# Optimization experiments

Measured on AMD Instinct MI355X. Metric: run time of the kernel, lower is better.

Reference implementation:

```python
import jax, jax.numpy as jnp
import numpy as np

DIM, HEADS, EMB = 768, 16, 1024
DH = DIM // HEADS                 # 48, divisible by 3 for 3D RoPE
T, RES = 3, 24
KT, KH, KW = 3, 5, 5              # neighborhood kernel
MLP = 4 * DIM
EPS = 1e-5


def _ln(x, w=None, b=None):
    m = x.mean(-1, keepdims=True)
    v = x.var(-1, keepdims=True)
    y = (x - m) * jax.lax.rsqrt(v + EPS)
    if w is not None:
        y = y * w + b
    return y


def _rope_cos_sin():
    # 3D axial RoPE: dim_head split into 3 equal chunks (t, h, w axes)
    da = DH // 3
    half = da // 2
    inv = 1.0 / (10000.0 ** (jnp.arange(half, dtype=jnp.float32) * 2.0 / da))
    def ang(n):
        return jnp.arange(n, dtype=jnp.float32)[:, None] * inv[None, :]  # (n, half)
    at, ah, aw = ang(T), ang(RES), ang(RES)
    A = jnp.concatenate([
        jnp.broadcast_to(at[:, None, None, :], (T, RES, RES, half)),
        jnp.broadcast_to(ah[None, :, None, :], (T, RES, RES, half)),
        jnp.broadcast_to(aw[None, None, :, :], (T, RES, RES, half)),
    ], axis=-1).reshape(T * RES * RES, DH // 2)
    return jnp.cos(A), jnp.sin(A)


def _rope(x, cos, sin):  # x: (B, nh, THW, DH); interleaved pair rotation
    x1, x2 = x[..., 0::2], x[..., 1::2]
    o1 = x1 * cos - x2 * sin
    o2 = x1 * sin + x2 * cos
    return jnp.stack([o1, o2], axis=-1).reshape(x.shape)


def _nbr(n, k):
    # NATTEN window: centered, shifted inward at borders (always exactly k neighbors)
    start = jnp.clip(jnp.arange(n) - k // 2, 0, n - k)
    return start[:, None] + jnp.arange(k)  # (n, k)


def setup_inputs():
    key = jax.random.key(0)
    ks = jax.random.split(key, 8)
    r = lambda k, s: jax.random.normal(k, s, dtype=jnp.float32) * 0.02
    return {
        "x": jax.random.normal(ks[0], (T, DIM, RES, RES), dtype=jnp.float32),
        "emb": jax.random.normal(ks[1], (T, EMB), dtype=jnp.float32),
        "w_mod": r(ks[2], (EMB, 2 * DIM)),
        "b_mod": jnp.zeros((2 * DIM,), jnp.float32),
        "qn_w": jnp.ones((DH,), jnp.float32),
        "qn_b": jnp.zeros((DH,), jnp.float32),
        "kn_w": jnp.ones((DH,), jnp.float32),
        "kn_b": jnp.zeros((DH,), jnp.float32),
        "W_fused": r(ks[3], (DIM, 3 * DIM + MLP)),
        "b_fused": jnp.zeros((3 * DIM + MLP,), jnp.float32),
        "W_out": r(ks[4], (DIM, DIM)),
        "W_mlp": r(ks[5], (MLP, DIM)),
        "b_mlp": jnp.zeros((DIM,), jnp.float32),
    }


def reference(x, emb, w_mod, b_mod, qn_w, qn_b, kn_w, kn_b,
              W_fused, b_fused, W_out, W_mlp, b_mlp):
    B = x.shape[0] // T
    H = W = RES
    THW = T * H * W
    x5 = x.reshape(B, T, DIM, H, W)
    skip = jnp.transpose(x5, (0, 1, 3, 4, 2))          # (B,T,H,W,C)
    xf = skip.reshape(B, THW, DIM)
    # conditioning emb repeated over spatial positions
    embr = jnp.repeat(emb.reshape(B, T, EMB)[:, :, None, :], H * W, axis=2)
    embr = embr.reshape(B, THW, EMB)
    # NormalizeWithCond: LayerNorm (no affine) + AdaLN modulation from emb
    mod = jax.nn.silu(embr) @ w_mod + b_mod
    scale, shift = jnp.split(mod, 2, axis=-1)
    h = _ln(xf) * (1.0 + scale) + shift
    # fused QKV + MLP projection
    fused = h @ W_fused + b_fused
    qkv, mlp_h = fused[..., :3 * DIM], fused[..., 3 * DIM:]
    qkv = qkv.reshape(B, THW, 3, HEADS, DH).transpose(2, 0, 3, 1, 4)  # (3,B,nh,THW,d)
    q, k, v = qkv[0], qkv[1], qkv[2]
    q = _ln(q, qn_w, qn_b)
    k = _ln(k, kn_w, kn_b)
    cos, sin = _rope_cos_sin()
    q = _rope(q, cos, sin)
    k = _rope(k, cos, sin)
    q = q.reshape(B, HEADS, T, H, W, DH) * (DH ** -0.5)
    k = k.reshape(B, HEADS, T, H, W, DH)
    v = v.reshape(B, HEADS, T, H, W, DH)
    it, ih, iw = _nbr(T, KT), _nbr(H, KH), _nbr(W, KW)
    def gather(z):  # -> (B,nh,T,KT,H,KH,W,KW,d)
        return z[:, :, it][:, :, :, :, ih][:, :, :, :, :, :, iw]
    kg, vg = gather(k), gather(v)
    attn = jnp.einsum('bnthwd,bntahcwed->bnthwace', q, kg)
    attn = jax.nn.softmax(attn.reshape(B, HEADS, T, H, W, KT * KH * KW), axis=-1)
    attn = attn.reshape(B, HEADS, T, H, W, KT, KH, KW)
    xa = jnp.einsum('bnthwace,bntahcwed->bnthwd', attn, vg)
    xa = jnp.transpose(xa, (0, 2, 3, 4, 1, 5)).reshape(B, T, H, W, DIM)
    y = skip + xa @ W_out
    y = y.reshape(B, THW, DIM) + (jax.nn.silu(mlp_h) @ W_mlp + b_mlp)
    y = jnp.transpose(y.reshape(B, T, H, W, DIM), (0, 1, 4, 2, 3))
    return y.reshape(B * T, DIM, H, W)
```

## Files before the change

kernel.cpp:

```cpp
#include <hip/hip_runtime.h>
#include <hip/hip_bf16.h>
#include <math.h>

#define T_    3
#define RES_  24
#define DIM_  768
#define HEADS_ 16
#define DH_   48
#define EMB_  1024
#define HW_   576
#define THW_  1728
#define MP_   1792
#define MLP_  3072
#define NF_   5376
#define QKV_  2304
#define KTOT_ 3840
#define SPLITK_ 6
#define EPS_  1e-5f

typedef __attribute__((ext_vector_type(8))) short bf16x8;
typedef __attribute__((ext_vector_type(4))) float f32x4;

__device__ __forceinline__ float siluf(float x) { return x / (1.f + expf(-x)); }

__device__ __forceinline__ unsigned short f2bf(float f) {
    __hip_bfloat16 b = __float2bfloat16(f);
    return *reinterpret_cast<unsigned short*>(&b);
}

__device__ __forceinline__ float bf2f(unsigned short u) {
    return __uint_as_float(((unsigned)u) << 16);
}

__device__ __forceinline__ void async_copy16(const void* g, void* l) {
    __builtin_amdgcn_global_load_lds(
        (__attribute__((address_space(1))) void*)g,
        (__attribute__((address_space(3))) void*)l,
        16, 0, 0);
}

__global__ __launch_bounds__(256) void conv_wfused_kernel(
    const float* __restrict__ W, unsigned short* __restrict__ Wt)
{
    __shared__ float tile[32][33];
    int n0 = blockIdx.x * 32;
    int k0 = blockIdx.y * 32;
    int c = threadIdx.x & 31;
    int r = threadIdx.x >> 5;
#pragma unroll
    for (int i = 0; i < 4; ++i)
        tile[r + 8 * i][c] = W[(size_t)(k0 + r + 8 * i) * NF_ + n0 + c];
    __syncthreads();
#pragma unroll
    for (int i = 0; i < 4; ++i)
        Wt[(size_t)(n0 + r + 8 * i) * DIM_ + k0 + c] = f2bf(tile[c][r + 8 * i]);
}

__global__ __launch_bounds__(256) void conv_wcat_kernel(
    const float* __restrict__ W_out, const float* __restrict__ W_mlp,
    unsigned short* __restrict__ Wt)
{
    __shared__ float tile[32][33];
    int k0 = blockIdx.x * 32;
    int n0 = blockIdx.y * 32;
    int c = threadIdx.x & 31;
    int r = threadIdx.x >> 5;
#pragma unroll
    for (int i = 0; i < 4; ++i) {
        int k = k0 + r + 8 * i;
        float v = (k < DIM_) ? W_out[(size_t)k * DIM_ + n0 + c]
                             : W_mlp[(size_t)(k - DIM_) * DIM_ + n0 + c];
        tile[r + 8 * i][c] = v;
    }
    __syncthreads();
#pragma unroll
    for (int i = 0; i < 4; ++i)
        Wt[(size_t)(n0 + r + 8 * i) * KTOT_ + k0 + c] = f2bf(tile[c][r + 8 * i]);
}

__global__ __launch_bounds__(256) void mod_kernel(
    const float* __restrict__ emb, const float* __restrict__ w_mod,
    const float* __restrict__ b_mod, float* __restrict__ mod)
{
    int t = blockIdx.y;
    int chunk = blockIdx.x;
    __shared__ float se[EMB_];
    __shared__ float part[128];
    int tid = threadIdx.x;
    for (int i = tid; i < EMB_; i += 256) {
        float e = emb[t * EMB_ + i];
        se[i] = e / (1.f + expf(-e));
    }
    __syncthreads();
    int r = tid >> 7;
    int c = tid & 127;
    int j = chunk * 128 + c;
    const float* wp = w_mod + j;
    float acc = 0.f;
    for (int e = r * 512; e < r * 512 + 512; ++e)
        acc += se[e] * wp[e * 1536];
    if (r == 1) part[c] = acc;
    __syncthreads();
    if (r == 0)
        mod[t * 1536 + j] = acc + part[c] + b_mod[j];
}

__global__ __launch_bounds__(256) void ln_mod_kernel(
    const float* __restrict__ x, const float* __restrict__ mod,
    unsigned short* __restrict__ h)
{
    int m = blockIdx.x;
    int t = m / HW_;
    int hw = m - t * HW_;
    const float* xp = x + (size_t)t * DIM_ * HW_ + hw;
    int tid = threadIdx.x;
    float v0 = xp[(size_t)tid * HW_];
    float v1 = xp[(size_t)(tid + 256) * HW_];
    float v2 = xp[(size_t)(tid + 512) * HW_];
    float s  = v0 + v1 + v2;
    float sq = v0 * v0 + v1 * v1 + v2 * v2;
#pragma unroll
    for (int off = 32; off > 0; off >>= 1) {
        s  += __shfl_xor(s, off, 64);
        sq += __shfl_xor(sq, off, 64);
    }
    __shared__ float ssum[4], ssq[4];
    int lane = tid & 63, wid = tid >> 6;
    if (lane == 0) { ssum[wid] = s; ssq[wid] = sq; }
    __syncthreads();
    float tot  = ssum[0] + ssum[1] + ssum[2] + ssum[3];
    float totq = ssq[0] + ssq[1] + ssq[2] + ssq[3];
    float mean = tot * (1.f / 768.f);
    float var  = totq * (1.f / 768.f) - mean * mean;
    float rs = rsqrtf(var + EPS_);
    const float* sc = mod + t * 1536;
    const float* sh = sc + 768;
    unsigned short* hp = h + (size_t)m * DIM_;
    hp[tid]       = f2bf((v0 - mean) * rs * (1.f + sc[tid])       + sh[tid]);
    hp[tid + 256] = f2bf((v1 - mean) * rs * (1.f + sc[tid + 256]) + sh[tid + 256]);
    hp[tid + 512] = f2bf((v2 - mean) * rs * (1.f + sc[tid + 512]) + sh[tid + 512]);
}

__global__ __launch_bounds__(256) void gemm1_kernel(
    const unsigned short* __restrict__ A,
    const unsigned short* __restrict__ Bt,
    const float* __restrict__ bias,
    float* __restrict__ qkv,
    unsigned short* __restrict__ A2)
{
    const int K = DIM_;
    __shared__ unsigned short As[128 * 32];
    __shared__ unsigned short Bs[128 * 32];
    int tid = threadIdx.x;
    int bm = blockIdx.y * 128;
    int bn = blockIdx.x * 128;
    int wave = tid >> 6, lane = tid & 63;
    int quad = lane >> 4, l16 = lane & 15;
    int wm = (wave & 1) * 64;
    int wn = (wave >> 1) * 64;
    f32x4 acc[4][4] = {};
    int srow = tid >> 2;
    int skk  = (tid & 3) * 8;
    const unsigned short* Ag = A + (size_t)(bm + srow) * K + skk;
    const unsigned short* Bg = Bt + (size_t)(bn + srow) * K + skk;
    unsigned short* la0 = &As[srow * 32 + skk];
    unsigned short* la1 = &As[(srow + 64) * 32 + skk];
    unsigned short* lb0 = &Bs[srow * 32 + skk];
    unsigned short* lb1 = &Bs[(srow + 64) * 32 + skk];
    for (int k0 = 0; k0 < K; k0 += 32) {
        async_copy16(Ag + k0, la0);
        async_copy16(Ag + (size_t)64 * K + k0, la1);
        async_copy16(Bg + k0, lb0);
        async_copy16(Bg + (size_t)64 * K + k0, lb1);
        __syncthreads();
        bf16x8 af[4], bf[4];
#pragma unroll
        for (int mt = 0; mt < 4; ++mt)
            af[mt] = *(const bf16x8*)&As[(wm + mt * 16 + l16) * 32 + quad * 8];
#pragma unroll
        for (int nt = 0; nt < 4; ++nt)
            bf[nt] = *(const bf16x8*)&Bs[(wn + nt * 16 + l16) * 32 + quad * 8];
#pragma unroll
        for (int mt = 0; mt < 4; ++mt)
#pragma unroll
            for (int nt = 0; nt < 4; ++nt)
                acc[mt][nt] = __builtin_amdgcn_mfma_f32_16x16x32_bf16(
                    af[mt], bf[nt], acc[mt][nt], 0, 0, 0);
        __syncthreads();
    }
#pragma unroll
    for (int mt = 0; mt < 4; ++mt) {
#pragma unroll
        for (int nt = 0; nt < 4; ++nt) {
            int gcol = bn + wn + nt * 16 + l16;
            float b = bias[gcol];
#pragma unroll
            for (int r = 0; r < 4; ++r) {
                int grow = bm + wm + mt * 16 + quad * 4 + r;
                if (grow < THW_) {
                    float v = acc[mt][nt][r] + b;
                    if (gcol < QKV_)
                        qkv[(size_t)grow * QKV_ + gcol] = v;
                    else
                        A2[(size_t)grow * KTOT_ + (gcol - QKV_ + DIM_)] = f2bf(siluf(v));
                }
            }
        }
    }
}

__global__ __launch_bounds__(256) void qkln_rope_kernel(
    const float* __restrict__ qkv,
    const float* __restrict__ qn_w, const float* __restrict__ qn_b,
    const float* __restrict__ kn_w, const float* __restrict__ kn_b,
    float* __restrict__ qb, float* __restrict__ kb)
{
    int tid = threadIdx.x;
    int lane = tid & 63, wid = tid >> 6;
    int idx = blockIdx.x * 4 + wid;
    int head = idx / THW_;
    int m = idx - head * THW_;
    const float* fp = qkv + (size_t)m * QKV_ + head * DH_;
    float qv = 0.f, kv = 0.f;
    if (lane < DH_) { qv = fp[lane]; kv = fp[768 + lane]; }
    float s = qv, sq = qv * qv, sk = kv, sqk = kv * kv;
#pragma unroll
    for (int off = 32; off > 0; off >>= 1) {
        s   += __shfl_xor(s, off, 64);
        sq  += __shfl_xor(sq, off, 64);
        sk  += __shfl_xor(sk, off, 64);
        sqk += __shfl_xor(sqk, off, 64);
    }
    float mq = s  * (1.f / 48.f), vq = sq  * (1.f / 48.f) - mq * mq;
    float mk = sk * (1.f / 48.f), vk = sqk * (1.f / 48.f) - mk * mk;
    float qn = 0.f, kn = 0.f;
    if (lane < DH_) {
        qn = (qv - mq) * rsqrtf(vq + EPS_) * qn_w[lane] + qn_b[lane];
        kn = (kv - mk) * rsqrtf(vk + EPS_) * kn_w[lane] + kn_b[lane];
    }
    int t = m / HW_; int hw = m - t * HW_;
    int hh = hw / RES_; int ww = hw - hh * RES_;
    int i = lane >> 1;
    int grp = i >> 3, j = i & 7;
    float pos = (grp == 0) ? (float)t : (grp == 1) ? (float)hh : (float)ww;
    float invf = exp2f(-1.6609640474436813f * (float)j);
    float ang = pos * invf;
    float cs = cosf(ang), sn = sinf(ang);
    float qp = __shfl_xor(qn, 1, 64);
    float kp = __shfl_xor(kn, 1, 64);
    float qo, ko;
    if ((lane & 1) == 0) { qo = qn * cs - qp * sn; ko = kn * cs - kp * sn; }
    else                 { qo = qp * sn + qn * cs; ko = kp * sn + kn * cs; }
    if (lane < DH_) {
        size_t o = ((size_t)head * THW_ + m) * DH_ + lane;
        qb[o] = qo * 0.14433756729740643f;
        kb[o] = ko;
    }
}

__global__ __launch_bounds__(256) void attn_kernel(
    const float* __restrict__ qb, const float* __restrict__ kb,
    const float* __restrict__ qkv, unsigned short* __restrict__ A2)
{
    __shared__ unsigned short Ks[144 * 72];
    __shared__ unsigned short Vt[48 * 168];
    __shared__ unsigned short Ps[64 * 168];

    int tid = threadIdx.x;
    int lane = tid & 63, wave = tid >> 6;
    int quad = lane >> 4, l16 = lane & 15;

    int head = blockIdx.x / 27;
    int tile = blockIdx.x - head * 27;
    int tt = tile / 9;
    int sp = tile - tt * 9;
    int h0 = (sp / 3) * 8;
    int w0 = (sp - (sp / 3) * 3) * 8;
    int u0h = min(max(h0 - 2, 0), RES_ - 12);
    int u0w = min(max(w0 - 2, 0), RES_ - 12);

    const float* qbh = qb + (size_t)head * THW_ * DH_;
    const float* kbh = kb + (size_t)head * THW_ * DH_;

    for (int i = tid; i < 144 * 24; i += 256) {
        int r = i / 24;
        Ks[r * 72 + 48 + (i - r * 24)] = 0;
    }
    for (int i = tid; i < 48 * 24; i += 256) {
        int r = i / 24;
        Vt[r * 168 + 144 + (i - r * 24)] = 0;
    }
    for (int i = tid; i < 64 * 24; i += 256) {
        int r = i / 24;
        Ps[r * 168 + 144 + (i - r * 24)] = 0;
    }

    int qbase = wave * 16;
    bf16x8 qf0, qf1;
    {
        int g = qbase + l16;
        int qtok = tt * HW_ + (h0 + (g >> 3)) * RES_ + (w0 + (g & 7));
        const float* qp = qbh + (size_t)qtok * DH_;
#pragma unroll
        for (int i = 0; i < 8; ++i) qf0[i] = (short)f2bf(qp[quad * 8 + i]);
        if (quad < 2) {
#pragma unroll
            for (int i = 0; i < 8; ++i) qf1[i] = (short)f2bf(qp[32 + quad * 8 + i]);
        } else {
#pragma unroll
            for (int i = 0; i < 8; ++i) qf1[i] = 0;
        }
    }

    int vmask[4];
#pragma unroll
    for (int r = 0; r < 4; ++r) {
        int g = qbase + quad * 4 + r;
        int qh = h0 + (g >> 3), qw = w0 + (g & 7);
        int hs = min(max(qh - 2, 0), RES_ - 5);
        int ws = min(max(qw - 2, 0), RES_ - 5);
        int vm = 0;
#pragma unroll
        for (int nt = 0; nt < 9; ++nt) {
            int kk = nt * 16 + l16;
            int hc = u0h + kk / 12;
            int wc = u0w + kk - (kk / 12) * 12;
            int ok = (hc >= hs) & (hc < hs + 5) & (wc >= ws) & (wc < ws + 5);
            vm |= ok << nt;
        }
        vmask[r] = vm;
    }

    float mrow[4] = {-1e30f, -1e30f, -1e30f, -1e30f};
    float lrow[4] = {};
    f32x4 Oacc[3] = {};

    for (int a = 0; a < T_; ++a) {
        for (int i = tid; i < 144 * 48; i += 256) {
            int kk = i / 48;
            int d = i - kk * 48;
            int hc = u0h + kk / 12;
            int wc = u0w + kk - (kk / 12) * 12;
            int tok = a * HW_ + hc * RES_ + wc;
            Ks[kk * 72 + d] = f2bf(kbh[(size_t)tok * DH_ + d]);
            Vt[d * 168 + kk] =
                f2bf(qkv[(size_t)tok * QKV_ + 1536 + head * DH_ + d]);
        }
        __syncthreads();

        f32x4 sc[9];
#pragma unroll
        for (int nt = 0; nt < 9; ++nt) {
            bf16x8 kf0 = *(const bf16x8*)&Ks[(nt * 16 + l16) * 72 + quad * 8];
            bf16x8 kf1 = *(const bf16x8*)&Ks[(nt * 16 + l16) * 72 + 32 + quad * 8];
            f32x4 z = {};
            z = __builtin_amdgcn_mfma_f32_16x16x32_bf16(qf0, kf0, z, 0, 0, 0);
            sc[nt] = __builtin_amdgcn_mfma_f32_16x16x32_bf16(qf1, kf1, z, 0, 0, 0);
        }

        float rmax[4] = {-1e30f, -1e30f, -1e30f, -1e30f};
#pragma unroll
        for (int nt = 0; nt < 9; ++nt)
#pragma unroll
            for (int r = 0; r < 4; ++r) {
                float s = ((vmask[r] >> nt) & 1) ? sc[nt][r] : -1e30f;
                sc[nt][r] = s;
                rmax[r] = fmaxf(rmax[r], s);
            }
#pragma unroll
        for (int off = 1; off < 16; off <<= 1)
#pragma unroll
            for (int r = 0; r < 4; ++r)
                rmax[r] = fmaxf(rmax[r], __shfl_xor(rmax[r], off));
        float alpha[4], rsum[4] = {};
#pragma unroll
        for (int r = 0; r < 4; ++r) {
            float mn = fmaxf(mrow[r], rmax[r]);
            alpha[r] = expf(mrow[r] - mn);
            mrow[r] = mn;
        }
#pragma unroll
        for (int nt = 0; nt < 9; ++nt)
#pragma unroll
            for (int r = 0; r < 4; ++r) {
                float p = expf(sc[nt][r] - mrow[r]);
                rsum[r] += p;
                Ps[(qbase + quad * 4 + r) * 168 + nt * 16 + l16] = f2bf(p);
            }
#pragma unroll
        for (int off = 1; off < 16; off <<= 1)
#pragma unroll
            for (int r = 0; r < 4; ++r)
                rsum[r] += __shfl_xor(rsum[r], off);
#pragma unroll
        for (int r = 0; r < 4; ++r)
            lrow[r] = lrow[r] * alpha[r] + rsum[r];
#pragma unroll
        for (int vt = 0; vt < 3; ++vt)
#pragma unroll
            for (int r = 0; r < 4; ++r)
                Oacc[vt][r] *= alpha[r];

#pragma unroll
        for (int ks = 0; ks < 5; ++ks) {
            bf16x8 pf = *(const bf16x8*)&Ps[(qbase + l16) * 168 + ks * 32 + quad * 8];
#pragma unroll
            for (int vt = 0; vt < 3; ++vt) {
                bf16x8 vf = *(const bf16x8*)&Vt[(vt * 16 + l16) * 168 + ks * 32 + quad * 8];
                Oacc[vt] = __builtin_amdgcn_mfma_f32_16x16x32_bf16(pf, vf, Oacc[vt], 0, 0, 0);
            }
        }
        __syncthreads();
    }

#pragma unroll
    for (int r = 0; r < 4; ++r) {
        int g = qbase + quad * 4 + r;
        int m = tt * HW_ + (h0 + (g >> 3)) * RES_ + (w0 + (g & 7));
        float inv = 1.f / lrow[r];
#pragma unroll
        for (int vt = 0; vt < 3; ++vt) {
            int d = vt * 16 + l16;
            A2[(size_t)m * KTOT_ + head * DH_ + d] = f2bf(Oacc[vt][r] * inv);
        }
    }
}

__global__ __launch_bounds__(256) void gemm2_kernel(
    const unsigned short* __restrict__ A,
    const unsigned short* __restrict__ Bt,
    unsigned short* __restrict__ P)
{
    const int K = KTOT_;
    __shared__ unsigned short As[128 * 32];
    __shared__ unsigned short Bs[128 * 32];
    int tid = threadIdx.x;
    int bm = blockIdx.y * 128;
    int bn = blockIdx.x * 128;
    int ks = blockIdx.z * (KTOT_ / SPLITK_);
    int wave = tid >> 6, lane = tid & 63;
    int quad = lane >> 4, l16 = lane & 15;
    int wm = (wave & 1) * 64;
    int wn = (wave >> 1) * 64;
    f32x4 acc[4][4] = {};
    int srow = tid >> 2;
    int skk  = (tid & 3) * 8;
    const unsigned short* Ag = A + (size_t)(bm + srow) * K + skk;
    const unsigned short* Bg = Bt + (size_t)(bn + srow) * K + skk;
    unsigned short* la0 = &As[srow * 32 + skk];
    unsigned short* la1 = &As[(srow + 64) * 32 + skk];
    unsigned short* lb0 = &Bs[srow * 32 + skk];
    unsigned short* lb1 = &Bs[(srow + 64) * 32 + skk];
    for (int k0 = ks; k0 < ks + KTOT_ / SPLITK_; k0 += 32) {
        async_copy16(Ag + k0, la0);
        async_copy16(Ag + (size_t)64 * K + k0, la1);
        async_copy16(Bg + k0, lb0);
        async_copy16(Bg + (size_t)64 * K + k0, lb1);
        __syncthreads();
        bf16x8 af[4], bf[4];
#pragma unroll
        for (int mt = 0; mt < 4; ++mt)
            af[mt] = *(const bf16x8*)&As[(wm + mt * 16 + l16) * 32 + quad * 8];
#pragma unroll
        for (int nt = 0; nt < 4; ++nt)
            bf[nt] = *(const bf16x8*)&Bs[(wn + nt * 16 + l16) * 32 + quad * 8];
#pragma unroll
        for (int mt = 0; mt < 4; ++mt)
#pragma unroll
            for (int nt = 0; nt < 4; ++nt)
                acc[mt][nt] = __builtin_amdgcn_mfma_f32_16x16x32_bf16(
                    af[mt], bf[nt], acc[mt][nt], 0, 0, 0);
        __syncthreads();
    }
    unsigned short* Pp = P + (size_t)blockIdx.z * MP_ * DIM_;
#pragma unroll
    for (int mt = 0; mt < 4; ++mt) {
#pragma unroll
        for (int nt = 0; nt < 4; ++nt) {
            int gcol = bn + wn + nt * 16 + l16;
#pragma unroll
            for (int r = 0; r < 4; ++r) {
                int grow = bm + wm + mt * 16 + quad * 4 + r;
                if (grow < THW_)
                    Pp[(size_t)grow * DIM_ + gcol] = f2bf(acc[mt][nt][r]);
            }
        }
    }
}

__global__ __launch_bounds__(256) void reduce_out_kernel(
    const unsigned short* __restrict__ P, const float* __restrict__ x,
    const float* __restrict__ b_mlp, float* __restrict__ out)
{
    __shared__ float tile[32][65];
    int bm = blockIdx.x * 64;
    int bn = blockIdx.y * 32;
    int tid = threadIdx.x;
    int t = bm / HW_;
    int hw0 = bm - t * HW_;
    for (int i = tid; i < 512; i += 256) {
        int ml = i >> 3;
        int n4 = (i & 7) * 4;
        float s0 = 0.f, s1 = 0.f, s2 = 0.f, s3 = 0.f;
#pragma unroll
        for (int sI = 0; sI < SPLITK_; ++sI) {
            const unsigned short* pp =
                P + ((size_t)sI * MP_ + bm + ml) * DIM_ + bn + n4;
            ushort4 u = *(const ushort4*)pp;
            s0 += bf2f(u.x); s1 += bf2f(u.y);
            s2 += bf2f(u.z); s3 += bf2f(u.w);
        }
        tile[n4 + 0][ml] = s0;
        tile[n4 + 1][ml] = s1;
        tile[n4 + 2][ml] = s2;
        tile[n4 + 3][ml] = s3;
    }
    __syncthreads();
    for (int i = tid; i < 512; i += 256) {
        int n = i >> 4;
        int ms = (i & 15) * 4;
        int gn = bn + n;
        size_t base = ((size_t)t * DIM_ + gn) * HW_ + hw0 + ms;
        float bv = b_mlp[gn];
        float4 xv = *(const float4*)(x + base);
        float4 o;
        o.x = xv.x + bv + tile[n][ms + 0];
        o.y = xv.y + bv + tile[n][ms + 1];
        o.z = xv.z + bv + tile[n][ms + 2];
        o.w = xv.w + bv + tile[n][ms + 3];
        *(float4*)(out + base) = o;
    }
}

extern "C" void kernel_launch(void* const* d_in, const int* in_sizes, int n_in,
                              void* d_out, int out_size, void* d_ws, size_t ws_size,
                              hipStream_t stream) {
    const float* x       = (const float*)d_in[0];
    const float* emb     = (const float*)d_in[1];
    const float* w_mod   = (const float*)d_in[2];
    const float* b_mod   = (const float*)d_in[3];
    const float* qn_w    = (const float*)d_in[4];
    const float* qn_b    = (const float*)d_in[5];
    const float* kn_w    = (const float*)d_in[6];
    const float* kn_b    = (const float*)d_in[7];
    const float* W_fused = (const float*)d_in[8];
    const float* b_fused = (const float*)d_in[9];
    const float* W_out   = (const float*)d_in[10];
    const float* W_mlp   = (const float*)d_in[11];
    const float* b_mlp   = (const float*)d_in[12];
    float* out = (float*)d_out;

    char* w = (char*)d_ws;
    float* mod = (float*)w;            w += (size_t)4608 * 4;
    float* qkv = (float*)w;            w += (size_t)THW_ * QKV_ * 4;
    float* qb  = (float*)w;            w += (size_t)HEADS_ * THW_ * DH_ * 4;
    float* kb  = (float*)w;            w += (size_t)HEADS_ * THW_ * DH_ * 4;
    unsigned short* h   = (unsigned short*)w;  w += (size_t)MP_ * DIM_ * 2;
    unsigned short* A2  = (unsigned short*)w;  w += (size_t)MP_ * KTOT_ * 2;
    unsigned short* Bt1 = (unsigned short*)w;  w += (size_t)NF_ * DIM_ * 2;
    unsigned short* Bt2 = (unsigned short*)w;  w += (size_t)DIM_ * KTOT_ * 2;
    unsigned short* P   = (unsigned short*)w;  w += (size_t)SPLITK_ * MP_ * DIM_ * 2;

    conv_wfused_kernel<<<dim3(NF_ / 32, DIM_ / 32), 256, 0, stream>>>(W_fused, Bt1);
    conv_wcat_kernel<<<dim3(KTOT_ / 32, DIM_ / 32), 256, 0, stream>>>(W_out, W_mlp, Bt2);
    mod_kernel<<<dim3(12, 3), 256, 0, stream>>>(emb, w_mod, b_mod, mod);
    ln_mod_kernel<<<THW_, 256, 0, stream>>>(x, mod, h);
    gemm1_kernel<<<dim3(NF_ / 128, MP_ / 128), 256, 0, stream>>>(h, Bt1, b_fused, qkv, A2);
    qkln_rope_kernel<<<(HEADS_ * THW_) / 4, 256, 0, stream>>>(qkv, qn_w, qn_b, kn_w, kn_b, qb, kb);
    attn_kernel<<<HEADS_ * 27, 256, 0, stream>>>(qb, kb, qkv, A2);
    gemm2_kernel<<<dim3(DIM_ / 128, MP_ / 128, SPLITK_), 256, 0, stream>>>(A2, Bt2, P);
    reduce_out_kernel<<<dim3(THW_ / 64, DIM_ / 32), 256, 0, stream>>>(P, x, b_mlp, out);
}
```

Measured before the change: 247.6 us.

## Store V, Q, K intermediates as bf16 and vectorize LN and attention loads

```diff
diff --git a/kernel.cpp b/kernel.cpp
--- a/kernel.cpp
+++ b/kernel.cpp
@@ -14,6 +14,7 @@
 #define MLP_  3072
 #define NF_   5376
 #define QKV_  2304
+#define QK_   1536
 #define KTOT_ 3840
 #define SPLITK_ 6
 #define EPS_  1e-5f
@@ -109,36 +110,58 @@
     const float* __restrict__ x, const float* __restrict__ mod,
     unsigned short* __restrict__ h)
 {
-    int m = blockIdx.x;
-    int t = m / HW_;
-    int hw = m - t * HW_;
-    const float* xp = x + (size_t)t * DIM_ * HW_ + hw;
+    int m0 = blockIdx.x * 4;
+    int t = m0 / HW_;
+    int hw0 = m0 - t * HW_;
+    const float* xp = x + (size_t)t * DIM_ * HW_ + hw0;
     int tid = threadIdx.x;
-    float v0 = xp[(size_t)tid * HW_];
-    float v1 = xp[(size_t)(tid + 256) * HW_];
-    float v2 = xp[(size_t)(tid + 512) * HW_];
-    float s  = v0 + v1 + v2;
-    float sq = v0 * v0 + v1 * v1 + v2 * v2;
+    float4 X0 = *(const float4*)(xp + (size_t)tid * HW_);
+    float4 X1 = *(const float4*)(xp + (size_t)(tid + 256) * HW_);
+    float4 X2 = *(const float4*)(xp + (size_t)(tid + 512) * HW_);
+    float4 sv, sqv;
+    sv.x = X0.x + X1.x + X2.x;  sv.y = X0.y + X1.y + X2.y;
+    sv.z = X0.z + X1.z + X2.z;  sv.w = X0.w + X1.w + X2.w;
+    sqv.x = X0.x*X0.x + X1.x*X1.x + X2.x*X2.x;
+    sqv.y = X0.y*X0.y + X1.y*X1.y + X2.y*X2.y;
+    sqv.z = X0.z*X0.z + X1.z*X1.z + X2.z*X2.z;
+    sqv.w = X0.w*X0.w + X1.w*X1.w + X2.w*X2.w;
 #pragma unroll
     for (int off = 32; off > 0; off >>= 1) {
-        s  += __shfl_xor(s, off, 64);
-        sq += __shfl_xor(sq, off, 64);
-    }
-    __shared__ float ssum[4], ssq[4];
+        sv.x += __shfl_xor(sv.x, off, 64);  sv.y += __shfl_xor(sv.y, off, 64);
+        sv.z += __shfl_xor(sv.z, off, 64);  sv.w += __shfl_xor(sv.w, off, 64);
+        sqv.x += __shfl_xor(sqv.x, off, 64); sqv.y += __shfl_xor(sqv.y, off, 64);
+        sqv.z += __shfl_xor(sqv.z, off, 64); sqv.w += __shfl_xor(sqv.w, off, 64);
+    }
+    __shared__ float4 ssum[4], ssq[4];
     int lane = tid & 63, wid = tid >> 6;
-    if (lane == 0) { ssum[wid] = s; ssq[wid] = sq; }
+    if (lane == 0) { ssum[wid] = sv; ssq[wid] = sqv; }
     __syncthreads();
-    float tot  = ssum[0] + ssum[1] + ssum[2] + ssum[3];
-    float totq = ssq[0] + ssq[1] + ssq[2] + ssq[3];
-    float mean = tot * (1.f / 768.f);
-    float var  = totq * (1.f / 768.f) - mean * mean;
-    float rs = rsqrtf(var + EPS_);
+    float mean[4], rs[4];
+#pragma unroll
+    for (int j = 0; j < 4; ++j) {
+        float tot  = ((const float*)&ssum[0])[j] + ((const float*)&ssum[1])[j]
+                   + ((const float*)&ssum[2])[j] + ((const float*)&ssum[3])[j];
+        float totq = ((const float*)&ssq[0])[j] + ((const float*)&ssq[1])[j]
+                   + ((const float*)&ssq[2])[j] + ((const float*)&ssq[3])[j];
+        float mn = tot * (1.f / 768.f);
+        float var = totq * (1.f / 768.f) - mn * mn;
+        mean[j] = mn;
+        rs[j] = rsqrtf(var + EPS_);
+    }
     const float* sc = mod + t * 1536;
     const float* sh = sc + 768;
-    unsigned short* hp = h + (size_t)m * DIM_;
-    hp[tid]       = f2bf((v0 - mean) * rs * (1.f + sc[tid])       + sh[tid]);
-    hp[tid + 256] = f2bf((v1 - mean) * rs * (1.f + sc[tid + 256]) + sh[tid + 256]);
-    hp[tid + 512] = f2bf((v2 - mean) * rs * (1.f + sc[tid + 512]) + sh[tid + 512]);
+#pragma unroll
+    for (int cc = 0; cc < 3; ++cc) {
+        int c = tid + cc * 256;
+        float4 X = (cc == 0) ? X0 : (cc == 1) ? X1 : X2;
+        float scl = 1.f + sc[c];
+        float shf = sh[c];
+        const float* Xp = (const float*)&X;
+#pragma unroll
+        for (int j = 0; j < 4; ++j)
+            h[(size_t)(m0 + j) * DIM_ + c] =
+                f2bf((Xp[j] - mean[j]) * rs[j] * scl + shf);
+    }
 }
 
 __global__ __launch_bounds__(256) void gemm1_kernel(
@@ -146,6 +169,7 @@
     const unsigned short* __restrict__ Bt,
     const float* __restrict__ bias,
     float* __restrict__ qkv,
+    unsigned short* __restrict__ vb,
     unsigned short* __restrict__ A2)
 {
     const int K = DIM_;
@@ -199,8 +223,10 @@
                 int grow = bm + wm + mt * 16 + quad * 4 + r;
                 if (grow < THW_) {
                     float v = acc[mt][nt][r] + b;
-                    if (gcol < QKV_)
-                        qkv[(size_t)grow * QKV_ + gcol] = v;
+                    if (gcol < QK_)
+                        qkv[(size_t)grow * QK_ + gcol] = v;
+                    else if (gcol < QKV_)
+                        vb[(size_t)grow * DIM_ + (gcol - QK_)] = f2bf(v);
                     else
                         A2[(size_t)grow * KTOT_ + (gcol - QKV_ + DIM_)] = f2bf(siluf(v));
                 }
@@ -213,14 +239,14 @@
     const float* __restrict__ qkv,
     const float* __restrict__ qn_w, const float* __restrict__ qn_b,
     const float* __restrict__ kn_w, const float* __restrict__ kn_b,
-    float* __restrict__ qb, float* __restrict__ kb)
+    unsigned short* __restrict__ qb, unsigned short* __restrict__ kb)
 {
     int tid = threadIdx.x;
     int lane = tid & 63, wid = tid >> 6;
     int idx = blockIdx.x * 4 + wid;
     int head = idx / THW_;
     int m = idx - head * THW_;
-    const float* fp = qkv + (size_t)m * QKV_ + head * DH_;
+    const float* fp = qkv + (size_t)m * QK_ + head * DH_;
     float qv = 0.f, kv = 0.f;
     if (lane < DH_) { qv = fp[lane]; kv = fp[768 + lane]; }
     float s = qv, sq = qv * qv, sk = kv, sqk = kv * kv;
@@ -253,14 +279,14 @@
     else                 { qo = qp * sn + qn * cs; ko = kp * sn + kn * cs; }
     if (lane < DH_) {
         size_t o = ((size_t)head * THW_ + m) * DH_ + lane;
-        qb[o] = qo * 0.14433756729740643f;
-        kb[o] = ko;
+        qb[o] = f2bf(qo * 0.14433756729740643f);
+        kb[o] = f2bf(ko);
     }
 }
 
 __global__ __launch_bounds__(256) void attn_kernel(
-    const float* __restrict__ qb, const float* __restrict__ kb,
-    const float* __restrict__ qkv, unsigned short* __restrict__ A2)
+    const unsigned short* __restrict__ qb, const unsigned short* __restrict__ kb,
+    const unsigned short* __restrict__ vb, unsigned short* __restrict__ A2)
 {
     __shared__ unsigned short Ks[144 * 72];
     __shared__ unsigned short Vt[48 * 168];
@@ -279,8 +305,9 @@
     int u0h = min(max(h0 - 2, 0), RES_ - 12);
     int u0w = min(max(w0 - 2, 0), RES_ - 12);
 
-    const float* qbh = qb + (size_t)head * THW_ * DH_;
-    const float* kbh = kb + (size_t)head * THW_ * DH_;
+    const unsigned short* qbh = qb + (size_t)head * THW_ * DH_;
+    const unsigned short* kbh = kb + (size_t)head * THW_ * DH_;
+    const unsigned short* vbh = vb + head * DH_;
 
     for (int i = tid; i < 144 * 24; i += 256) {
         int r = i / 24;
@@ -300,13 +327,10 @@
     {
         int g = qbase + l16;
         int qtok = tt * HW_ + (h0 + (g >> 3)) * RES_ + (w0 + (g & 7));
-        const float* qp = qbh + (size_t)qtok * DH_;
-#pragma unroll
-        for (int i = 0; i < 8; ++i) qf0[i] = (short)f2bf(qp[quad * 8 + i]);
-        if (quad < 2) {
-#pragma unroll
-            for (int i = 0; i < 8; ++i) qf1[i] = (short)f2bf(qp[32 + quad * 8 + i]);
-        } else {
+        const unsigned short* qp = qbh + (size_t)qtok * DH_;
+        qf0 = *(const bf16x8*)(qp + quad * 8);
+        if (quad < 2) qf1 = *(const bf16x8*)(qp + 32 + quad * 8);
+        else {
 #pragma unroll
             for (int i = 0; i < 8; ++i) qf1[i] = 0;
         }
@@ -336,15 +360,19 @@
     f32x4 Oacc[3] = {};
 
     for (int a = 0; a < T_; ++a) {
-        for (int i = tid; i < 144 * 48; i += 256) {
-            int kk = i / 48;
-            int d = i - kk * 48;
+        for (int i = tid; i < 144 * 12; i += 256) {
+            int kk = i / 12;
+            int g = i - kk * 12;
             int hc = u0h + kk / 12;
             int wc = u0w + kk - (kk / 12) * 12;
             int tok = a * HW_ + hc * RES_ + wc;
-            Ks[kk * 72 + d] = f2bf(kbh[(size_t)tok * DH_ + d]);
-            Vt[d * 168 + kk] =
-                f2bf(qkv[(size_t)tok * QKV_ + 1536 + head * DH_ + d]);
+            ushort4 k4 = *(const ushort4*)(kbh + (size_t)tok * DH_ + 4 * g);
+            *(ushort4*)&Ks[kk * 72 + 4 * g] = k4;
+            ushort4 v4 = *(const ushort4*)(vbh + (size_t)tok * DIM_ + 4 * g);
+            Vt[(4 * g + 0) * 168 + kk] = v4.x;
+            Vt[(4 * g + 1) * 168 + kk] = v4.y;
+            Vt[(4 * g + 2) * 168 + kk] = v4.z;
+            Vt[(4 * g + 3) * 168 + kk] = v4.w;
         }
         __syncthreads();
 
@@ -552,9 +580,10 @@
 
     char* w = (char*)d_ws;
     float* mod = (float*)w;            w += (size_t)4608 * 4;
-    float* qkv = (float*)w;            w += (size_t)THW_ * QKV_ * 4;
-    float* qb  = (float*)w;            w += (size_t)HEADS_ * THW_ * DH_ * 4;
-    float* kb  = (float*)w;            w += (size_t)HEADS_ * THW_ * DH_ * 4;
+    float* qkv = (float*)w;            w += (size_t)THW_ * QK_ * 4;
+    unsigned short* vb  = (unsigned short*)w;  w += (size_t)THW_ * DIM_ * 2;
+    unsigned short* qb  = (unsigned short*)w;  w += (size_t)HEADS_ * THW_ * DH_ * 2;
+    unsigned short* kb  = (unsigned short*)w;  w += (size_t)HEADS_ * THW_ * DH_ * 2;
     unsigned short* h   = (unsigned short*)w;  w += (size_t)MP_ * DIM_ * 2;
     unsigned short* A2  = (unsigned short*)w;  w += (size_t)MP_ * KTOT_ * 2;
     unsigned short* Bt1 = (unsigned short*)w;  w += (size_t)NF_ * DIM_ * 2;
@@ -564,10 +593,10 @@
     conv_wfused_kernel<<<dim3(NF_ / 32, DIM_ / 32), 256, 0, stream>>>(W_fused, Bt1);
     conv_wcat_kernel<<<dim3(KTOT_ / 32, DIM_ / 32), 256, 0, stream>>>(W_out, W_mlp, Bt2);
     mod_kernel<<<dim3(12, 3), 256, 0, stream>>>(emb, w_mod, b_mod, mod);
-    ln_mod_kernel<<<THW_, 256, 0, stream>>>(x, mod, h);
-    gemm1_kernel<<<dim3(NF_ / 128, MP_ / 128), 256, 0, stream>>>(h, Bt1, b_fused, qkv, A2);
+    ln_mod_kernel<<<THW_ / 4, 256, 0, stream>>>(x, mod, h);
+    gemm1_kernel<<<dim3(NF_ / 128, MP_ / 128), 256, 0, stream>>>(h, Bt1, b_fused, qkv, vb, A2);
     qkln_rope_kernel<<<(HEADS_ * THW_) / 4, 256, 0, stream>>>(qkv, qn_w, qn_b, kn_w, kn_b, qb, kb);
-    attn_kernel<<<HEADS_ * 27, 256, 0, stream>>>(qb, kb, qkv, A2);
+    attn_kernel<<<HEADS_ * 27, 256, 0, stream>>>(qb, kb, vb, A2);
     gemm2_kernel<<<dim3(DIM_ / 128, MP_ / 128, SPLITK_), 256, 0, stream>>>(A2, Bt2, P);
     reduce_out_kernel<<<dim3(THW_ / 64, DIM_ / 32), 256, 0, stream>>>(P, x, b_mlp, out);
 }
```

Measured after the change: 238.0 us. 1.04x faster.
